# Optimization experiments

Measured on AMD Instinct MI355X. Metric: run time of the kernel, lower is better.

Reference implementation:

```python
import jax, jax.numpy as jnp
import numpy as np

DIM = 512
HEADS = 8
DEPTH = DIM // HEADS
DFF = 2048
EPS = 1e-3  # keras BatchNormalization default epsilon


def _dense_params(key, d_in, d_out, bias=True):
    k1, k2 = jax.random.split(key)
    lim = 1.0 / np.sqrt(d_in)
    W = jax.random.uniform(k1, (d_in, d_out), minval=-lim, maxval=lim, dtype=jnp.float32)
    if bias:
        b = jnp.zeros((d_out,), jnp.float32)
        return W, b
    return W


def _bn_params(key, d):
    k1, k2 = jax.random.split(key)
    gamma = 1.0 + 0.1 * jax.random.normal(k1, (d,), jnp.float32)
    beta = 0.1 * jax.random.normal(k2, (d,), jnp.float32)
    mean = 0.05 * jax.random.normal(jax.random.fold_in(key, 7), (d,), jnp.float32)
    var = jnp.ones((d,), jnp.float32)
    return gamma, beta, mean, var


def setup_inputs() -> dict:
    key = jax.random.key(0)
    ks = jax.random.split(key, 20)
    B, S_dec, S_enc = 32, 384, 384
    inp = {
        'enc_output': jax.random.normal(ks[0], (B, S_enc, DIM), jnp.float32),
        'x2': jax.random.normal(ks[1], (B, S_dec, DIM), jnp.float32),
    }
    # mha1 (self-attn) params
    for i, nm in enumerate(['q1', 'k1', 'v1', 'o1']):
        W, b = _dense_params(ks[2 + i], DIM, DIM)
        inp[f'W{nm}'], inp[f'b{nm}'] = W, b
    # mha2 (cross-attn) params
    for i, nm in enumerate(['q2', 'k2', 'v2', 'o2']):
        W, b = _dense_params(ks[6 + i], DIM, DIM)
        inp[f'W{nm}'], inp[f'b{nm}'] = W, b
    # FFN
    inp['Wff1'] = _dense_params(ks[10], DIM, DFF, bias=False)
    inp['Wff2'] = _dense_params(ks[11], DFF, DIM, bias=False)
    # 4 batchnorms
    for i in range(1, 5):
        g, be, m, v = _bn_params(ks[11 + i], DIM)
        inp[f'bn{i}_gamma'], inp[f'bn{i}_beta'] = g, be
        inp[f'bn{i}_mean'], inp[f'bn{i}_var'] = m, v
    return inp


def _split_heads(x):
    B, S, _ = x.shape
    return x.reshape(B, S, HEADS, DEPTH).transpose(0, 2, 1, 3)


def _mha(q_in, k_in, v_in, Wq, bq, Wk, bk, Wv, bv, Wo, bo, causal):
    q = _split_heads(q_in @ Wq + bq)
    k = _split_heads(k_in @ Wk + bk)
    v = _split_heads(v_in @ Wv + bv)
    logits = jnp.einsum('bhqd,bhkd->bhqk', q, k) / jnp.sqrt(jnp.float32(DEPTH))
    if causal:
        Sq, Sk = logits.shape[-2], logits.shape[-1]
        mask = jnp.tril(jnp.ones((Sq, Sk), bool))
        logits = jnp.where(mask, logits, jnp.finfo(logits.dtype).min)
    attn = jax.nn.softmax(logits, axis=-1)
    out = jnp.einsum('bhqk,bhkd->bhqd', attn, v)
    B, _, S, _ = out.shape
    out = out.transpose(0, 2, 1, 3).reshape(B, S, DIM)
    return out @ Wo + bo


def _bn(x, gamma, beta, mean, var):
    return (x - mean) * jax.lax.rsqrt(var + EPS) * gamma + beta


def reference(enc_output, x2,
              Wq1, bq1, Wk1, bk1, Wv1, bv1, Wo1, bo1,
              Wq2, bq2, Wk2, bk2, Wv2, bv2, Wo2, bo2,
              Wff1, Wff2,
              bn1_gamma, bn1_beta, bn1_mean, bn1_var,
              bn2_gamma, bn2_beta, bn2_mean, bn2_var,
              bn3_gamma, bn3_beta, bn3_mean, bn3_var,
              bn4_gamma, bn4_beta, bn4_mean, bn4_var):
    # self-attention with causal mask (dropout = identity)
    x = _mha(x2, x2, x2, Wq1, bq1, Wk1, bk1, Wv1, bv1, Wo1, bo1, causal=True)
    x = x + x2
    xn = _bn(x, bn1_gamma, bn1_beta, bn1_mean, bn1_var)
    y = _bn(enc_output, bn2_gamma, bn2_beta, bn2_mean, bn2_var)
    # cross-attention (no mask); residual adds x2 (as in source)
    x = _mha(xn, y, y, Wq2, bq2, Wk2, bk2, Wv2, bv2, Wo2, bo2, causal=False)
    x = x + x2
    cross_out = x
    x = _bn(x, bn3_gamma, bn3_beta, bn3_mean, bn3_var)
    x = jax.nn.relu(x @ Wff1) @ Wff2
    x = x + cross_out
    x = _bn(x, bn4_gamma, bn4_beta, bn4_mean, bn4_var)
    return x
```

## Files before the change

kernel.cpp:

```cpp
#include <hip/hip_runtime.h>
#include <cstdint>
#include <cstddef>

typedef __bf16 bf16;
typedef __bf16 bf16x8 __attribute__((ext_vector_type(8)));
typedef __bf16 bf16x4 __attribute__((ext_vector_type(4)));
typedef float  f32x4  __attribute__((ext_vector_type(4)));

#define B_   32
#define S_   384
#define D_   512
#define H_   8
#define DH_  64
#define DFF_ 2048
#define NTOK (B_*S_)

__device__ __forceinline__ void gload16(const void* g, void* l){
  __builtin_amdgcn_global_load_lds((__attribute__((address_space(1))) uint32_t*)(g),
                                   (__attribute__((address_space(3))) uint32_t*)(l), 16, 0, 0);
}

struct PrepArgs { const float* w8[8]; const float* wff1; const float* wff2; const float* bn[16]; };
__global__ __launch_bounds__(256) void prep_all(PrepArgs pa, bf16* Wt8, bf16* Wff1t, bf16* Wff2t,
                                                float* sc, float* sh){
  __shared__ float t[64][65];
  int id = blockIdx.x;
  if (id < 1024){
    const float* src; bf16* dst; int R, C, tr, tc;
    if (id < 512){
      int w = id >> 6, tl = id & 63;
      src = pa.w8[w]; dst = Wt8 + (size_t)w*262144; R = 512; C = 512;
      tr = (tl>>3)*64; tc = (tl&7)*64;
    } else if (id < 768){
      int tl = id - 512;
      src = pa.wff1; dst = Wff1t; R = 512; C = 2048;
      tr = (tl>>5)*64; tc = (tl&31)*64;
    } else {
      int tl = id - 768;
      src = pa.wff2; dst = Wff2t; R = 2048; C = 512;
      tr = (tl>>3)*64; tc = (tl&7)*64;
    }
    for (int i=threadIdx.x; i<4096; i+=256){ int r=i>>6, c=i&63; t[r][c] = src[(size_t)(tr+r)*C + tc+c]; }
    __syncthreads();
    for (int i=threadIdx.x; i<4096; i+=256){ int c=i>>6, r=i&63; dst[(size_t)(tc+c)*R + tr+r] = (bf16)t[r][c]; }
  } else {
    int t2 = id - 1024;
    int i = t2 >> 1, half = t2 & 1;
    int n = half*256 + threadIdx.x;
    float g = pa.bn[i*4+0][n], b = pa.bn[i*4+1][n], m = pa.bn[i*4+2][n], v = pa.bn[i*4+3][n];
    float s = g * rsqrtf(v + 1e-3f);
    sc[i*512+n] = s; sh[i*512+n] = b - m*s;
  }
}

__global__ __launch_bounds__(256) void cvt2(const float* __restrict__ enc, const float* __restrict__ x2,
                                            const float* __restrict__ sc, const float* __restrict__ sh,
                                            bf16* __restrict__ E2, bf16* __restrict__ X2b){
  size_t e0 = ((size_t)blockIdx.x*256 + threadIdx.x)*4;
  if (blockIdx.y == 0){
    int n0 = (int)(e0 & (D_-1));
    f32x4 xv = *(const f32x4*)(enc + e0);
    bf16x4 ov;
    #pragma unroll
    for (int j=0;j<4;j++) ov[j] = (bf16)(xv[j]*sc[n0+j] + sh[n0+j]);
    *(bf16x4*)(E2 + e0) = ov;
  } else {
    f32x4 xv = *(const f32x4*)(x2 + e0);
    bf16x4 ov;
    #pragma unroll
    for (int j=0;j<4;j++) ov[j] = (bf16)xv[j];
    *(bf16x4*)(X2b + e0) = ov;
  }
}

__global__ __launch_bounds__(256,3) void gemm_bt(
    const bf16* __restrict__ A, const bf16* __restrict__ Wt,
    const float* __restrict__ b0, const float* __restrict__ b1, const float* __restrict__ b2,
    const bf16* __restrict__ residb,
    const float* __restrict__ bsc, const float* __restrict__ bsh,
    bf16* __restrict__ o0, bf16* __restrict__ o1b,
    bf16* __restrict__ vt, int vseg,
    float* __restrict__ of, bf16* __restrict__ pre,
    int M, int N, int K, int relu, int mode)
{
  __shared__ bf16 As[2][64*64];
  __shared__ bf16 Bs[2][128*64];
  int nwg = gridDim.x;
  int cpx = nwg >> 3;
  int bid = blockIdx.x;
  int swz = (bid & 7)*cpx + (bid >> 3);
  int tiles_n = N >> 7;
  int tm = swz / tiles_n, tn = swz - tm*tiles_n;

  int tid = threadIdx.x, wave = tid>>6, lane = tid&63;
  int lhi = lane>>4, llo = lane&15;
  int lrow = lane>>3, lcol = lane&7;
  int wr = wave>>1, wc = wave&1;

  f32x4 acc[2][4];
  #pragma unroll
  for (int i=0;i<2;i++)
    #pragma unroll
    for (int j=0;j<4;j++) acc[i][j] = (f32x4){0.f,0.f,0.f,0.f};

  const bf16* Abase = A  + (size_t)(tm*64)  * K;
  const bf16* Bbase = Wt + (size_t)(tn*128) * K;

  int arow0 = wave*16, brow0 = wave*32;

  auto STAGE = [&](int buf, int kt){
    #pragma unroll
    for (int q=0;q<2;q++){
      int r = arow0 + q*8 + lrow;
      int s = lcol ^ (r&7);
      gload16(Abase + (size_t)r*K + kt + s*8, (char*)&As[buf][0] + wave*2048 + q*1024);
    }
    #pragma unroll
    for (int q=0;q<4;q++){
      int r = brow0 + q*8 + lrow;
      int s = lcol ^ (r&7);
      gload16(Bbase + (size_t)r*K + kt + s*8, (char*)&Bs[buf][0] + wave*4096 + q*1024);
    }
  };

  STAGE(0, 0);
  __syncthreads();
  int nt = K >> 6;
  int cur = 0;
  for (int t=0; t<nt; ++t){
    if (t+1 < nt) STAGE(cur^1, (t+1)<<6);
    #pragma unroll
    for (int ks=0; ks<2; ks++){
      bf16x8 af[2], bfr[4];
      #pragma unroll
      for (int i=0;i<2;i++){
        int row = wr*32 + i*16 + llo;
        int slot = (ks*4 + lhi) ^ (row&7);
        af[i] = *(const bf16x8*)&As[cur][row*64 + slot*8];
      }
      #pragma unroll
      for (int j=0;j<4;j++){
        int row = wc*64 + j*16 + llo;
        int slot = (ks*4 + lhi) ^ (row&7);
        bfr[j] = *(const bf16x8*)&Bs[cur][row*64 + slot*8];
      }
      #pragma unroll
      for (int i=0;i<2;i++)
        #pragma unroll
        for (int j=0;j<4;j++)
          acc[i][j] = __builtin_amdgcn_mfma_f32_16x16x32_bf16(af[i], bfr[j], acc[i][j], 0,0,0);
    }
    __syncthreads();
    cur ^= 1;
  }

  int m0 = tm*64 + wr*32, n0 = tn*128 + wc*64;
  #pragma unroll
  for (int i=0;i<2;i++){
    #pragma unroll
    for (int j=0;j<4;j++){
      int gn = n0 + j*16 + llo;
      float vv[4];
      #pragma unroll
      for (int rr=0;rr<4;rr++){
        int gm = m0 + i*16 + lhi*4 + rr;
        float v = acc[i][j][rr];
        if (b0){
          const float* bp = (gn < 512) ? b0 : ((gn < 1024) ? b1 : b2);
          v += bp[gn & 511];
        }
        if (residb) v += (float)residb[(size_t)gm*N + gn];
        vv[rr] = v;
      }
      int gm0 = m0 + i*16 + lhi*4;
      if (mode == 1){
        int seg = gn >> 9, cn = gn & 511;
        int h = cn >> 6, dd = cn & 63;
        int bb = gm0 / S_, ss0 = gm0 - bb*S_;
        if (seg == vseg){
          bf16x4 v4;
          #pragma unroll
          for (int rr=0;rr<4;rr++) v4[rr] = (bf16)vv[rr];
          *(bf16x4*)&vt[((size_t)(bb*H_ + h)*DH_ + dd)*S_ + ss0] = v4;
        } else {
          bf16* hp = (seg == 0) ? o0 : o1b;
          #pragma unroll
          for (int rr=0;rr<4;rr++)
            hp[(((size_t)(bb*H_ + h))*S_ + ss0 + rr)*DH_ + dd] = (bf16)vv[rr];
        }
      } else {
        #pragma unroll
        for (int rr=0;rr<4;rr++){
          int gm = gm0 + rr;
          float v = vv[rr];
          if (pre)  pre[(size_t)gm*N + gn] = (bf16)v;
          if (bsc)  v = v*bsc[gn & 511] + bsh[gn & 511];
          if (relu) v = fmaxf(v, 0.f);
          if (of) of[(size_t)gm*N + gn] = v;
          else    o0[(size_t)gm*N + gn] = (bf16)v;
        }
      }
    }
  }
}

__global__ __launch_bounds__(256,4) void gemm_bt2(
    const bf16* __restrict__ A, const bf16* __restrict__ Wt,
    const float* __restrict__ b0, const float* __restrict__ b1, const float* __restrict__ b2,
    const bf16* __restrict__ residb,
    bf16* __restrict__ o0, bf16* __restrict__ o1b,
    bf16* __restrict__ vt, int vseg,
    int M, int N, int K, int relu, int mode)
{
  __shared__ bf16 As[2][128*32];
  __shared__ bf16 Bs[2][128*32];
  int nwg = gridDim.x;
  int cpx = nwg >> 3;
  int bid = blockIdx.x;
  int swz = (bid & 7)*cpx + (bid >> 3);
  int tiles_n = N >> 7;
  int tm = swz / tiles_n, tn = swz - tm*tiles_n;

  int tid = threadIdx.x, wave = tid>>6, lane = tid&63;
  int lhi = lane>>4, llo = lane&15;
  int srow = lane>>2, sslot = lane&3;
  int wr = wave>>1, wc = wave&1;

  f32x4 acc[4][4];
  #pragma unroll
  for (int i=0;i<4;i++)
    #pragma unroll
    for (int j=0;j<4;j++) acc[i][j] = (f32x4){0.f,0.f,0.f,0.f};

  const bf16* Abase = A  + (size_t)(tm*128) * K;
  const bf16* Bbase = Wt + (size_t)(tn*128) * K;

  auto STAGE = [&](int buf, int kt){
    #pragma unroll
    for (int q=0;q<2;q++){
      int r = wave*32 + q*16 + srow;
      int s = sslot ^ ((r>>1)&3);
      gload16(Abase + (size_t)r*K + kt + s*8, (char*)&As[buf][0] + wave*2048 + q*1024);
    }
    #pragma unroll
    for (int q=0;q<2;q++){
      int r = wave*32 + q*16 + srow;
      int s = sslot ^ ((r>>1)&3);
      gload16(Bbase + (size_t)r*K + kt + s*8, (char*)&Bs[buf][0] + wave*2048 + q*1024);
    }
  };

  STAGE(0, 0);
  __syncthreads();
  int nt = K >> 5;
  int cur = 0;
  for (int t=0; t<nt; ++t){
    if (t+1 < nt) STAGE(cur^1, (t+1)<<5);
    bf16x8 af[4], bfr[4];
    #pragma unroll
    for (int i=0;i<4;i++){
      int row = wr*64 + i*16 + llo;
      int slot = lhi ^ ((row>>1)&3);
      af[i] = *(const bf16x8*)&As[cur][row*32 + slot*8];
    }
    #pragma unroll
    for (int j=0;j<4;j++){
      int row = wc*64 + j*16 + llo;
      int slot = lhi ^ ((row>>1)&3);
      bfr[j] = *(const bf16x8*)&Bs[cur][row*32 + slot*8];
    }
    #pragma unroll
    for (int i=0;i<4;i++)
      #pragma unroll
      for (int j=0;j<4;j++)
        acc[i][j] = __builtin_amdgcn_mfma_f32_16x16x32_bf16(af[i], bfr[j], acc[i][j], 0,0,0);
    __syncthreads();
    cur ^= 1;
  }

  int m0 = tm*128 + wr*64, n0 = tn*128 + wc*64;
  #pragma unroll
  for (int i=0;i<4;i++){
    #pragma unroll
    for (int j=0;j<4;j++){
      int gn = n0 + j*16 + llo;
      float vv[4];
      #pragma unroll
      for (int rr=0;rr<4;rr++){
        int gm = m0 + i*16 + lhi*4 + rr;
        float v = acc[i][j][rr];
        if (b0){
          const float* bp = (gn < 512) ? b0 : ((gn < 1024) ? b1 : b2);
          v += bp[gn & 511];
        }
        if (residb) v += (float)residb[(size_t)gm*N + gn];
        vv[rr] = v;
      }
      int gm0 = m0 + i*16 + lhi*4;
      if (mode == 1){
        int seg = gn >> 9, cn = gn & 511;
        int h = cn >> 6, dd = cn & 63;
        int bb = gm0 / S_, ss0 = gm0 - bb*S_;
        if (seg == vseg){
          bf16x4 v4;
          #pragma unroll
          for (int rr=0;rr<4;rr++) v4[rr] = (bf16)vv[rr];
          *(bf16x4*)&vt[((size_t)(bb*H_ + h)*DH_ + dd)*S_ + ss0] = v4;
        } else {
          bf16* hp = (seg == 0) ? o0 : o1b;
          #pragma unroll
          for (int rr=0;rr<4;rr++)
            hp[(((size_t)(bb*H_ + h))*S_ + ss0 + rr)*DH_ + dd] = (bf16)vv[rr];
        }
      } else {
        #pragma unroll
        for (int rr=0;rr<4;rr++){
          int gm = gm0 + rr;
          float v = vv[rr];
          if (relu) v = fmaxf(v, 0.f);
          o0[(size_t)gm*N + gn] = (bf16)v;
        }
      }
    }
  }
}

__global__ __launch_bounds__(256,4) void attn(
    const bf16* __restrict__ Q, const bf16* __restrict__ Kx,
    const bf16* __restrict__ Vt, bf16* __restrict__ out, int causal)
{
  __shared__ bf16 Ks[2][64*64];
  __shared__ bf16 Vs[2][64*64];
  __shared__ bf16 Ps[4][16*64];
  int bid = blockIdx.x;
  int bh = bid & 255;
  int qb = bid >> 8;
  int b = bh >> 3, h = bh & 7;
  int tid = threadIdx.x, wave = tid>>6, lane = tid&63;
  int lhi = lane>>4, llo = lane&15;
  int l7 = llo & 7;
  const bf16* Qb = Q  + (size_t)bh*S_*DH_;
  const bf16* Kb = Kx + (size_t)bh*S_*DH_;
  const bf16* Vb = Vt + (size_t)bh*DH_*S_;

  bf16x8 qf[2];
  #pragma unroll
  for (int f=0; f<2; f++)
    qf[f] = *(const bf16x8*)&Qb[(size_t)(qb*64 + wave*16 + llo)*DH_ + f*32 + lhi*8];

  f32x4 oacc[4];
  #pragma unroll
  for (int f=0; f<4; f++) oacc[f] = (f32x4){0.f,0.f,0.f,0.f};
  float mrow[4], lrow4[4];
  #pragma unroll
  for (int r=0;r<4;r++){ mrow[r] = -1e9f; lrow4[r] = 0.f; }

  int KT = causal ? (qb+1) : (S_/64);

  int srow0 = tid>>3, sslot = tid&7;
  bf16x8 krA[2], vrA[2], krB[2], vrB[2];

  auto ISSUE = [&](bf16x8 (&KR)[2], bf16x8 (&VR)[2], int kb){
    const bf16* kt0 = Kb + (size_t)kb*64*DH_;
    #pragma unroll
    for (int s=0;s<2;s++){
      int row = s*32 + srow0;
      KR[s] = *(const bf16x8*)&kt0[(size_t)row*64 + sslot*8];
      VR[s] = *(const bf16x8*)&Vb[(size_t)row*S_ + (size_t)kb*64 + sslot*8];
    }
  };
  auto COMMIT = [&](bf16x8 (&KR)[2], bf16x8 (&VR)[2], int buf){
    #pragma unroll
    for (int s=0;s<2;s++){
      int row = s*32 + srow0;
      int sl = sslot ^ (row&7);
      *(bf16x8*)&Ks[buf][row*64 + sl*8] = KR[s];
      *(bf16x8*)&Vs[buf][row*64 + sl*8] = VR[s];
    }
  };

  ISSUE(krA, vrA, 0);
  COMMIT(krA, vrA, 0);
  if (KT > 1) ISSUE(krB, vrB, 1);

  for (int kb=0; kb<KT; kb++){
    int buf = kb & 1;
    __syncthreads();

    f32x4 sc[4];
    #pragma unroll
    for (int f=0; f<4; f++){
      f32x4 z = (f32x4){0.f,0.f,0.f,0.f};
      #pragma unroll
      for (int ks=0; ks<2; ks++){
        int row = f*16 + llo;
        int slot = (ks*4 + lhi) ^ (row&7);
        bf16x8 kf = *(const bf16x8*)&Ks[buf][row*64 + slot*8];
        z = __builtin_amdgcn_mfma_f32_16x16x32_bf16(qf[ks], kf, z, 0,0,0);
      }
      sc[f] = z;
    }
    #pragma unroll
    for (int f=0; f<4; f++)
      #pragma unroll
      for (int r=0;r<4;r++){
        float v = sc[f][r]*0.125f;
        if (causal && kb==KT-1){
          int gcol = kb*64 + f*16 + llo;
          int grow = qb*64 + wave*16 + lhi*4 + r;
          if (gcol > grow) v = -1e9f;
        }
        sc[f][r] = v;
      }

    float alpha[4], psum[4];
    #pragma unroll
    for (int r=0;r<4;r++){
      float vm = fmaxf(fmaxf(sc[0][r],sc[1][r]), fmaxf(sc[2][r],sc[3][r]));
      #pragma unroll
      for (int msk=1; msk<16; msk<<=1) vm = fmaxf(vm, __shfl_xor(vm, msk));
      float mn = fmaxf(mrow[r], vm);
      alpha[r] = __expf(mrow[r]-mn);
      mrow[r]  = mn;
      psum[r]  = 0.f;
    }
    #pragma unroll
    for (int f=0; f<4; f++)
      #pragma unroll
      for (int r=0;r<4;r++){
        float p = __expf(sc[f][r]-mrow[r]);
        psum[r] += p;
        int row = lhi*4 + r;
        int slot = (f*2 + (llo>>3)) ^ (row&7);
        Ps[wave][row*64 + slot*8 + l7] = (bf16)p;
      }
    #pragma unroll
    for (int r=0;r<4;r++){
      float s = psum[r];
      #pragma unroll
      for (int msk=1; msk<16; msk<<=1) s += __shfl_xor(s, msk);
      lrow4[r] = lrow4[r]*alpha[r] + s;
      #pragma unroll
      for (int f=0; f<4; f++) oacc[f][r] *= alpha[r];
    }

    if (kb+2 < KT){
      if ((kb & 1) == 0) ISSUE(krA, vrA, kb+2);
      else               ISSUE(krB, vrB, kb+2);
    }

    asm volatile("s_waitcnt lgkmcnt(0)" ::: "memory");
    __builtin_amdgcn_sched_barrier(0);

    #pragma unroll
    for (int ks=0; ks<2; ks++){
      int pslot = (ks*4 + lhi) ^ l7;
      bf16x8 pf = *(const bf16x8*)&Ps[wave][llo*64 + pslot*8];
      #pragma unroll
      for (int f2=0; f2<4; f2++){
        int row = f2*16 + llo;
        int slot = (ks*4 + lhi) ^ (row&7);
        bf16x8 vf = *(const bf16x8*)&Vs[buf][row*64 + slot*8];
        oacc[f2] = __builtin_amdgcn_mfma_f32_16x16x32_bf16(pf, vf, oacc[f2], 0,0,0);
      }
    }

    if (kb+1 < KT){
      if ((kb & 1) == 0) COMMIT(krB, vrB, buf^1);
      else               COMMIT(krA, vrA, buf^1);
    }
  }

  int qg = qb*64 + wave*16;
  #pragma unroll
  for (int f2=0; f2<4; f2++)
    #pragma unroll
    for (int r=0;r<4;r++){
      int row = qg + lhi*4 + r;
      int dd  = f2*16 + llo;
      out[((size_t)(b*S_ + row))*D_ + h*DH_ + dd] = (bf16)(oacc[f2][r] / lrow4[r]);
    }
}

extern "C" void kernel_launch(void* const* d_in, const int* in_sizes, int n_in,
                              void* d_out, int out_size, void* d_ws, size_t ws_size,
                              hipStream_t stream)
{
  (void)in_sizes; (void)n_in; (void)out_size; (void)ws_size;
  const float* enc = (const float*)d_in[0];
  const float* x2  = (const float*)d_in[1];
  const float* bq1 = (const float*)d_in[3];
  const float* bk1 = (const float*)d_in[5];
  const float* bv1 = (const float*)d_in[7];
  const float* bo1 = (const float*)d_in[9];
  const float* bq2 = (const float*)d_in[11];
  const float* bk2 = (const float*)d_in[13];
  const float* bv2 = (const float*)d_in[15];
  const float* bo2 = (const float*)d_in[17];
  float* outp = (float*)d_out;

  char* ws = (char*)d_ws;
  size_t off = 0;
  auto alloc = [&](size_t bytes)->void*{ void* p = ws + off; off += (bytes+255)&~(size_t)255; return p; };
  bf16* Wt8   = (bf16*)alloc((size_t)8*512*512*2);
  bf16* Wff1t = (bf16*)alloc((size_t)DFF_*D_*2);
  bf16* Wff2t = (bf16*)alloc((size_t)D_*DFF_*2);
  float* bnsc = (float*)alloc(4*512*4);
  float* bnsh = (float*)alloc(4*512*4);
  size_t actB = (size_t)NTOK*D_*2;
  bf16* X2b  = (bf16*)alloc(actB);
  bf16* Abuf = (bf16*)alloc(actB);
  bf16* Bbuf = (bf16*)alloc(actB);
  bf16* Cbuf = (bf16*)alloc(actB);
  bf16* Dv   = (bf16*)alloc(actB);
  bf16* E1   = (bf16*)alloc(actB);
  bf16* E2   = (bf16*)alloc(actB);
  bf16* E3   = E2;
  bf16* Fbuf = Abuf;

  bf16* Wtq1 = Wt8 + 0*262144;
  bf16* Wto1 = Wt8 + 3*262144;
  bf16* Wtq2 = Wt8 + 4*262144;
  bf16* Wtk2 = Wt8 + 5*262144;
  bf16* Wto2 = Wt8 + 7*262144;

  PrepArgs pa;
  pa.w8[0]=(const float*)d_in[2];  pa.w8[1]=(const float*)d_in[4];
  pa.w8[2]=(const float*)d_in[6];  pa.w8[3]=(const float*)d_in[8];
  pa.w8[4]=(const float*)d_in[10]; pa.w8[5]=(const float*)d_in[12];
  pa.w8[6]=(const float*)d_in[14]; pa.w8[7]=(const float*)d_in[16];
  pa.wff1=(const float*)d_in[18];  pa.wff2=(const float*)d_in[19];
  for (int i=0;i<16;i++) pa.bn[i] = (const float*)d_in[20+i];
  prep_all<<<1032,256,0,stream>>>(pa, Wt8, Wff1t, Wff2t, bnsc, bnsh);
  cvt2<<<dim3(NTOK*D_/4/256, 2),256,0,stream>>>(enc, x2, bnsc+512, bnsh+512, E2, X2b);

  auto gemm = [&](const bf16* Am, const bf16* W,
                  const float* bb0, const float* bb1, const float* bb2,
                  const bf16* residb, const float* sc, const float* sh,
                  bf16* oo0, bf16* oo1, bf16* vt, int vseg,
                  float* of, bf16* pre,
                  int N, int K, int relu, int mode){
    gemm_bt<<<(NTOK/64)*(N/128), 256, 0, stream>>>(Am, W, bb0, bb1, bb2, residb, sc, sh,
                                                   oo0, oo1, vt, vseg, of, pre,
                                                   NTOK, N, K, relu, mode);
  };
  auto gemm2 = [&](const bf16* Am, const bf16* W,
                   const float* bb0, const float* bb1, const float* bb2,
                   bf16* oo0, bf16* oo1, bf16* vt, int vseg,
                   int N, int K, int relu, int mode){
    gemm_bt2<<<(NTOK/128)*(N/128), 256, 0, stream>>>(Am, W, bb0, bb1, bb2, nullptr,
                                                     oo0, oo1, vt, vseg,
                                                     NTOK, N, K, relu, mode);
  };

  gemm2(X2b, Wtq1, bq1, bk1, bv1, Abuf, Bbuf, Dv, 2, 1536, 512, 0, 1);
  attn<<<(S_/64)*B_*H_, 256, 0, stream>>>(Abuf, Bbuf, Dv, Cbuf, 1);
  gemm(Cbuf, Wto1, bo1, nullptr, nullptr, X2b, bnsc+0, bnsh+0,
       E1, nullptr, nullptr, -1, nullptr, nullptr, 512, 512, 0, 0);

  gemm(E1, Wtq2, bq2, nullptr, nullptr, nullptr, nullptr, nullptr,
       Abuf, nullptr, nullptr, -1, nullptr, nullptr, 512, 512, 0, 1);
  gemm2(E2, Wtk2, bk2, bv2, nullptr, Bbuf, nullptr, Dv, 1, 1024, 512, 0, 1);
  attn<<<(S_/64)*B_*H_, 256, 0, stream>>>(Abuf, Bbuf, Dv, Cbuf, 0);
  gemm(Cbuf, Wto2, bo2, nullptr, nullptr, X2b, bnsc+2*512, bnsh+2*512,
       E1, nullptr, nullptr, -1, nullptr, E3, 512, 512, 0, 0);

  gemm2(E1, Wff1t, nullptr, nullptr, nullptr, Fbuf, nullptr, nullptr, -1, DFF_, 512, 1, 0);
  gemm(Fbuf, Wff2t, nullptr, nullptr, nullptr, E3, bnsc+3*512, bnsh+3*512,
       nullptr, nullptr, nullptr, -1, outp, nullptr, 512, DFF_, 0, 0);
}
```

Before: 327.4 us.

## Triple-buffer gemm_bt2, fuse cross-attn Q/KV projections, single-buffer attention

gemm_bt2 gets a three-stage LDS ring with explicit vmcnt waits and one barrier per k-step. It also gains an optional second A source chosen by N-tile, so the cross-attention Q and K/V projections run as one 1536-wide launch. The FFN2 GEMM moves to the 128x128 gemm_bt2 with BN and fp32 output support. The attention kernel drops its register double-buffering of K/V for a single LDS buffer plus an extra barrier, trading latency hiding for lower LDS use and register pressure.

```diff
diff --git a/kernel.cpp b/kernel.cpp
--- a/kernel.cpp
+++ b/kernel.cpp
@@ -75,7 +75,7 @@
 
 __global__ __launch_bounds__(256,3) void gemm_bt(
     const bf16* __restrict__ A, const bf16* __restrict__ Wt,
-    const float* __restrict__ b0, const float* __restrict__ b1, const float* __restrict__ b2,
+    const float* __restrict__ b0,
     const bf16* __restrict__ residb,
     const float* __restrict__ bsc, const float* __restrict__ bsh,
     bf16* __restrict__ o0, bf16* __restrict__ o1b,
@@ -165,10 +165,7 @@
       for (int rr=0;rr<4;rr++){
         int gm = m0 + i*16 + lhi*4 + rr;
         float v = acc[i][j][rr];
-        if (b0){
-          const float* bp = (gn < 512) ? b0 : ((gn < 1024) ? b1 : b2);
-          v += bp[gn & 511];
-        }
+        if (b0) v += b0[gn & 511];
         if (residb) v += (float)residb[(size_t)gm*N + gn];
         vv[rr] = v;
       }
@@ -204,16 +201,19 @@
   }
 }
 
-__global__ __launch_bounds__(256,4) void gemm_bt2(
-    const bf16* __restrict__ A, const bf16* __restrict__ Wt,
+__global__ __launch_bounds__(256,3) void gemm_bt2(
+    const bf16* __restrict__ A, const bf16* __restrict__ A2, int tnA,
+    const bf16* __restrict__ Wt,
     const float* __restrict__ b0, const float* __restrict__ b1, const float* __restrict__ b2,
     const bf16* __restrict__ residb,
+    const float* __restrict__ bsc, const float* __restrict__ bsh,
     bf16* __restrict__ o0, bf16* __restrict__ o1b,
     bf16* __restrict__ vt, int vseg,
+    float* __restrict__ of,
     int M, int N, int K, int relu, int mode)
 {
-  __shared__ bf16 As[2][128*32];
-  __shared__ bf16 Bs[2][128*32];
+  __shared__ bf16 As[3][128*32];
+  __shared__ bf16 Bs[3][128*32];
   int nwg = gridDim.x;
   int cpx = nwg >> 3;
   int bid = blockIdx.x;
@@ -232,8 +232,9 @@
     #pragma unroll
     for (int j=0;j<4;j++) acc[i][j] = (f32x4){0.f,0.f,0.f,0.f};
 
-  const bf16* Abase = A  + (size_t)(tm*128) * K;
-  const bf16* Bbase = Wt + (size_t)(tn*128) * K;
+  const bf16* Asrc = (A2 && tn >= tnA) ? A2 : A;
+  const bf16* Abase = Asrc + (size_t)(tm*128) * K;
+  const bf16* Bbase = Wt   + (size_t)(tn*128) * K;
 
   auto STAGE = [&](int buf, int kt){
     #pragma unroll
@@ -250,12 +251,19 @@
     }
   };
 
+  int nt = K >> 5;
   STAGE(0, 0);
-  __syncthreads();
-  int nt = K >> 5;
-  int cur = 0;
+  STAGE(1, 32);
+  int cur = 0, st = 2;
   for (int t=0; t<nt; ++t){
-    if (t+1 < nt) STAGE(cur^1, (t+1)<<5);
+    if (t+1 < nt) asm volatile("s_waitcnt vmcnt(4)" ::: "memory");
+    else          asm volatile("s_waitcnt vmcnt(0)" ::: "memory");
+    __builtin_amdgcn_s_barrier();
+    asm volatile("" ::: "memory");
+    if (t+2 < nt){
+      STAGE(st, (t+2)<<5);
+      st = (st==2) ? 0 : st+1;
+    }
     bf16x8 af[4], bfr[4];
     #pragma unroll
     for (int i=0;i<4;i++){
@@ -274,8 +282,7 @@
       #pragma unroll
       for (int j=0;j<4;j++)
         acc[i][j] = __builtin_amdgcn_mfma_f32_16x16x32_bf16(af[i], bfr[j], acc[i][j], 0,0,0);
-    __syncthreads();
-    cur ^= 1;
+    cur = (cur==2) ? 0 : cur+1;
   }
 
   int m0 = tm*128 + wr*64, n0 = tn*128 + wc*64;
@@ -317,8 +324,10 @@
         for (int rr=0;rr<4;rr++){
           int gm = gm0 + rr;
           float v = vv[rr];
+          if (bsc)  v = v*bsc[gn & 511] + bsh[gn & 511];
           if (relu) v = fmaxf(v, 0.f);
-          o0[(size_t)gm*N + gn] = (bf16)v;
+          if (of) of[(size_t)gm*N + gn] = v;
+          else    o0[(size_t)gm*N + gn] = (bf16)v;
         }
       }
     }
@@ -329,8 +338,8 @@
     const bf16* __restrict__ Q, const bf16* __restrict__ Kx,
     const bf16* __restrict__ Vt, bf16* __restrict__ out, int causal)
 {
-  __shared__ bf16 Ks[2][64*64];
-  __shared__ bf16 Vs[2][64*64];
+  __shared__ bf16 Ks[64*64];
+  __shared__ bf16 Vs[64*64];
   __shared__ bf16 Ps[4][16*64];
   int bid = blockIdx.x;
   int bh = bid & 255;
@@ -358,33 +367,27 @@
   int KT = causal ? (qb+1) : (S_/64);
 
   int srow0 = tid>>3, sslot = tid&7;
-  bf16x8 krA[2], vrA[2], krB[2], vrB[2];
-
-  auto ISSUE = [&](bf16x8 (&KR)[2], bf16x8 (&VR)[2], int kb){
+  bf16x8 kreg[2], vreg[2];
+
+  auto issue = [&](int kb){
     const bf16* kt0 = Kb + (size_t)kb*64*DH_;
     #pragma unroll
     for (int s=0;s<2;s++){
       int row = s*32 + srow0;
-      KR[s] = *(const bf16x8*)&kt0[(size_t)row*64 + sslot*8];
-      VR[s] = *(const bf16x8*)&Vb[(size_t)row*S_ + (size_t)kb*64 + sslot*8];
+      kreg[s] = *(const bf16x8*)&kt0[(size_t)row*64 + sslot*8];
+      vreg[s] = *(const bf16x8*)&Vb[(size_t)row*S_ + (size_t)kb*64 + sslot*8];
     }
   };
-  auto COMMIT = [&](bf16x8 (&KR)[2], bf16x8 (&VR)[2], int buf){
+  issue(0);
+
+  for (int kb=0; kb<KT; kb++){
     #pragma unroll
     for (int s=0;s<2;s++){
       int row = s*32 + srow0;
       int sl = sslot ^ (row&7);
-      *(bf16x8*)&Ks[buf][row*64 + sl*8] = KR[s];
-      *(bf16x8*)&Vs[buf][row*64 + sl*8] = VR[s];
-    }
-  };
-
-  ISSUE(krA, vrA, 0);
-  COMMIT(krA, vrA, 0);
-  if (KT > 1) ISSUE(krB, vrB, 1);
-
-  for (int kb=0; kb<KT; kb++){
-    int buf = kb & 1;
+      *(bf16x8*)&Ks[row*64 + sl*8] = kreg[s];
+      *(bf16x8*)&Vs[row*64 + sl*8] = vreg[s];
+    }
     __syncthreads();
 
     f32x4 sc[4];
@@ -395,7 +398,7 @@
       for (int ks=0; ks<2; ks++){
         int row = f*16 + llo;
         int slot = (ks*4 + lhi) ^ (row&7);
-        bf16x8 kf = *(const bf16x8*)&Ks[buf][row*64 + slot*8];
+        bf16x8 kf = *(const bf16x8*)&Ks[row*64 + slot*8];
         z = __builtin_amdgcn_mfma_f32_16x16x32_bf16(qf[ks], kf, z, 0,0,0);
       }
       sc[f] = z;
@@ -444,10 +447,7 @@
       for (int f=0; f<4; f++) oacc[f][r] *= alpha[r];
     }
 
-    if (kb+2 < KT){
-      if ((kb & 1) == 0) ISSUE(krA, vrA, kb+2);
-      else               ISSUE(krB, vrB, kb+2);
-    }
+    if (kb+1 < KT) issue(kb+1);
 
     asm volatile("s_waitcnt lgkmcnt(0)" ::: "memory");
     __builtin_amdgcn_sched_barrier(0);
@@ -460,15 +460,11 @@
       for (int f2=0; f2<4; f2++){
         int row = f2*16 + llo;
         int slot = (ks*4 + lhi) ^ (row&7);
-        bf16x8 vf = *(const bf16x8*)&Vs[buf][row*64 + slot*8];
+        bf16x8 vf = *(const bf16x8*)&Vs[row*64 + slot*8];
         oacc[f2] = __builtin_amdgcn_mfma_f32_16x16x32_bf16(pf, vf, oacc[f2], 0,0,0);
       }
     }
-
-    if (kb+1 < KT){
-      if ((kb & 1) == 0) COMMIT(krB, vrB, buf^1);
-      else               COMMIT(krA, vrA, buf^1);
-    }
+    __syncthreads();
   }
 
   int qg = qb*64 + wave*16;
@@ -521,7 +517,6 @@
   bf16* Wtq1 = Wt8 + 0*262144;
   bf16* Wto1 = Wt8 + 3*262144;
   bf16* Wtq2 = Wt8 + 4*262144;
-  bf16* Wtk2 = Wt8 + 5*262144;
   bf16* Wto2 = Wt8 + 7*262144;
 
   PrepArgs pa;
@@ -534,38 +529,35 @@
   prep_all<<<1032,256,0,stream>>>(pa, Wt8, Wff1t, Wff2t, bnsc, bnsh);
   cvt2<<<dim3(NTOK*D_/4/256, 2),256,0,stream>>>(enc, x2, bnsc+512, bnsh+512, E2, X2b);
 
-  auto gemm = [&](const bf16* Am, const bf16* W,
-                  const float* bb0, const float* bb1, const float* bb2,
+  auto gemm = [&](const bf16* Am, const bf16* W, const float* bb0,
                   const bf16* residb, const float* sc, const float* sh,
-                  bf16* oo0, bf16* oo1, bf16* vt, int vseg,
-                  float* of, bf16* pre,
-                  int N, int K, int relu, int mode){
-    gemm_bt<<<(NTOK/64)*(N/128), 256, 0, stream>>>(Am, W, bb0, bb1, bb2, residb, sc, sh,
-                                                   oo0, oo1, vt, vseg, of, pre,
-                                                   NTOK, N, K, relu, mode);
+                  bf16* oo0, float* of, bf16* pre, int N, int K, int relu){
+    gemm_bt<<<(NTOK/64)*(N/128), 256, 0, stream>>>(Am, W, bb0, residb, sc, sh,
+                                                   oo0, nullptr, nullptr, -1, of, pre,
+                                                   NTOK, N, K, relu, 0);
   };
-  auto gemm2 = [&](const bf16* Am, const bf16* W,
+  auto gemm2 = [&](const bf16* Am, const bf16* A2, int tnA, const bf16* W,
                    const float* bb0, const float* bb1, const float* bb2,
-                   bf16* oo0, bf16* oo1, bf16* vt, int vseg,
+                   const bf16* residb, const float* sc, const float* sh,
+                   bf16* oo0, bf16* oo1, bf16* vt, int vseg, float* of,
                    int N, int K, int relu, int mode){
-    gemm_bt2<<<(NTOK/128)*(N/128), 256, 0, stream>>>(Am, W, bb0, bb1, bb2, nullptr,
-                                                     oo0, oo1, vt, vseg,
+    gemm_bt2<<<(NTOK/128)*(N/128), 256, 0, stream>>>(Am, A2, tnA, W, bb0, bb1, bb2,
+                                                     residb, sc, sh, oo0, oo1, vt, vseg, of,
                                                      NTOK, N, K, relu, mode);
   };
 
-  gemm2(X2b, Wtq1, bq1, bk1, bv1, Abuf, Bbuf, Dv, 2, 1536, 512, 0, 1);
+  gemm2(X2b, nullptr, 0, Wtq1, bq1, bk1, bv1, nullptr, nullptr, nullptr,
+        Abuf, Bbuf, Dv, 2, nullptr, 1536, 512, 0, 1);
   attn<<<(S_/64)*B_*H_, 256, 0, stream>>>(Abuf, Bbuf, Dv, Cbuf, 1);
-  gemm(Cbuf, Wto1, bo1, nullptr, nullptr, X2b, bnsc+0, bnsh+0,
-       E1, nullptr, nullptr, -1, nullptr, nullptr, 512, 512, 0, 0);
-
-  gemm(E1, Wtq2, bq2, nullptr, nullptr, nullptr, nullptr, nullptr,
-       Abuf, nullptr, nullptr, -1, nullptr, nullptr, 512, 512, 0, 1);
-  gemm2(E2, Wtk2, bk2, bv2, nullptr, Bbuf, nullptr, Dv, 1, 1024, 512, 0, 1);
+  gemm(Cbuf, Wto1, bo1, X2b, bnsc+0, bnsh+0, E1, nullptr, nullptr, 512, 512, 0);
+
+  gemm2(E1, E2, 4, Wtq2, bq2, bk2, bv2, nullptr, nullptr, nullptr,
+        Abuf, Bbuf, Dv, 2, nullptr, 1536, 512, 0, 1);
   attn<<<(S_/64)*B_*H_, 256, 0, stream>>>(Abuf, Bbuf, Dv, Cbuf, 0);
-  gemm(Cbuf, Wto2, bo2, nullptr, nullptr, X2b, bnsc+2*512, bnsh+2*512,
-       E1, nullptr, nullptr, -1, nullptr, E3, 512, 512, 0, 0);
-
-  gemm2(E1, Wff1t, nullptr, nullptr, nullptr, Fbuf, nullptr, nullptr, -1, DFF_, 512, 1, 0);
-  gemm(Fbuf, Wff2t, nullptr, nullptr, nullptr, E3, bnsc+3*512, bnsh+3*512,
-       nullptr, nullptr, nullptr, -1, outp, nullptr, 512, DFF_, 0, 0);
-}
+  gemm(Cbuf, Wto2, bo2, X2b, bnsc+2*512, bnsh+2*512, E1, nullptr, E3, 512, 512, 0);
+
+  gemm2(E1, nullptr, 0, Wff1t, nullptr, nullptr, nullptr, nullptr, nullptr, nullptr,
+        Fbuf, nullptr, nullptr, -1, nullptr, DFF_, 512, 1, 0);
+  gemm2(Fbuf, nullptr, 0, Wff2t, nullptr, nullptr, nullptr, E3, bnsc+3*512, bnsh+3*512,
+        nullptr, nullptr, nullptr, -1, outp, 512, DFF_, 0, 0);
+}
```

New measurement: 334.9 us. 2.3% more time.
